# Optimization experiments

Hardware: AMD Instinct MI355X
Metric: run time of the kernel (lower is better)

Reference implementation:

```python
import jax, jax.numpy as jnp
import numpy as np

N = 50000      # nodes
E = 800000     # edges (before self loops)
IN, H, OUT = 128, 64, 64
NEG_SLOPE = 0.2  # PyG GATConv leaky_relu slope


def _glorot(k, shape):
    lim = float(np.sqrt(6.0 / (shape[0] + shape[1])))
    return jax.random.uniform(k, shape, jnp.float32, -lim, lim)


def setup_inputs() -> dict:
    key = jax.random.key(0)
    ks = jax.random.split(key, 16)
    x = jax.random.normal(ks[0], (N, IN), jnp.float32)
    edge_src = jax.random.randint(ks[1], (E,), 0, N, jnp.int32)
    edge_dst = jax.random.randint(ks[2], (E,), 0, N, jnp.int32)
    dims = [(IN, H), (H, H), (H, OUT)]
    inp = {"x": x, "edge_src": edge_src, "edge_dst": edge_dst}
    i = 3
    for l, (di, do) in enumerate(dims):
        inp[f"W{l}"] = _glorot(ks[i], (di, do)); i += 1
        inp[f"as{l}"] = _glorot(ks[i], (1, do))[0]; i += 1
        inp[f"ad{l}"] = _glorot(ks[i], (1, do))[0]; i += 1
        inp[f"b{l}"] = jnp.zeros((do,), jnp.float32)
    return inp


def _gat_layer(x, W, a_src, a_dst, b, src, dst):
    # single-head GATConv (PyG semantics, self loops already in src/dst)
    h = x @ W                              # [N, do]
    s = h @ a_src                          # [N] source attention logits
    d = h @ a_dst                          # [N] dest attention logits
    e = jax.nn.leaky_relu(s[src] + d[dst], NEG_SLOPE)   # [E']
    # segment softmax over incoming edges of each destination node
    m = jax.ops.segment_max(e, dst, num_segments=N)
    w = jnp.exp(e - m[dst])
    denom = jax.ops.segment_sum(w, dst, num_segments=N)
    coef = w / (denom[dst] + 1e-16)
    out = jax.ops.segment_sum(h[src] * coef[:, None], dst, num_segments=N)
    return out + b


def reference(x, edge_src, edge_dst, W0, as0, ad0, b0, W1, as1, ad1, b1, W2, as2, ad2, b2):
    # add self loops (GATConv default add_self_loops=True)
    loop = jnp.arange(N, dtype=edge_src.dtype)
    src = jnp.concatenate([edge_src, loop])
    dst = jnp.concatenate([edge_dst, loop])
    h = jax.nn.relu(_gat_layer(x, W0, as0, ad0, b0, src, dst))
    # dropout is identity in eval mode
    h = jax.nn.relu(_gat_layer(h, W1, as1, ad1, b1, src, dst))
    return _gat_layer(h, W2, as2, ad2, b2, src, dst)
```

## Files before the change

kernel.cpp:

```cpp
#include <hip/hip_runtime.h>
#include <math.h>

#define WAVE 64
#define NEG_SLOPE 0.2f


__global__ __launch_bounds__(256) void bucket_count_kernel(
    const int* __restrict__ dst, int* __restrict__ gcnt, int e, int nb) {
    extern __shared__ int cnt[];
    for (int b = threadIdx.x; b < nb; b += 256) cnt[b] = 0;
    __syncthreads();
    int base = blockIdx.x * 4096;
#pragma unroll
    for (int k = 0; k < 16; ++k) {
        int i = base + k * 256 + threadIdx.x;
        if (i < e) atomicAdd(&cnt[dst[i] >> 7], 1);
    }
    __syncthreads();
    for (int b = threadIdx.x; b < nb; b += 256) {
        int c = cnt[b];
        if (c) atomicAdd(&gcnt[b], c);
    }
}

__global__ __launch_bounds__(512) void bucket_scan_kernel(
    const int* __restrict__ gcnt, int* __restrict__ boff, int* __restrict__ gfill,
    int* __restrict__ rowptr, int nb, int e, int n) {
    __shared__ int sh[512];
    int t = threadIdx.x;
    int v = (t < nb) ? gcnt[t] : 0;
    sh[t] = v;
    __syncthreads();
    for (int o = 1; o < 512; o <<= 1) {
        int u = (t >= o) ? sh[t - o] : 0;
        __syncthreads();
        sh[t] += u;
        __syncthreads();
    }
    if (t < nb) { int ex = sh[t] - v; boff[t] = ex; gfill[t] = ex; }
    if (t == 0) { boff[nb] = e; rowptr[n] = e + n; }
}

__global__ __launch_bounds__(256) void bucket_place_kernel(
    const int* __restrict__ src, const int* __restrict__ dst,
    int* __restrict__ gfill, int2* __restrict__ binned, int e, int nb) {
    extern __shared__ int lds[];
    int* cnt = lds;
    int* bas = lds + nb;
    for (int b = threadIdx.x; b < nb; b += 256) cnt[b] = 0;
    __syncthreads();
    int base = blockIdx.x * 4096;
#pragma unroll
    for (int k = 0; k < 16; ++k) {
        int i = base + k * 256 + threadIdx.x;
        if (i < e) atomicAdd(&cnt[dst[i] >> 7], 1);
    }
    __syncthreads();
    for (int b = threadIdx.x; b < nb; b += 256) {
        int c = cnt[b];
        bas[b] = c ? atomicAdd(&gfill[b], c) : 0;
        cnt[b] = 0;
    }
    __syncthreads();
#pragma unroll
    for (int k = 0; k < 16; ++k) {
        int i = base + k * 256 + threadIdx.x;
        if (i < e) {
            int d = dst[i];
            int bk = d >> 7;
            int r = atomicAdd(&cnt[bk], 1);
            binned[bas[bk] + r] = make_int2(src[i], d);
        }
    }
}

__global__ __launch_bounds__(256) void bucket_build_kernel(
    const int2* __restrict__ binned, const int* __restrict__ boff,
    int* __restrict__ csr_src, int* __restrict__ rowptr, int n) {
    __shared__ int cnt[128], off[128], pcnt[128];
    int b = blockIdx.x;
    int t = threadIdx.x;
    int nodeBase = b << 7;
    int nc = min(128, n - nodeBase);
    int e0 = boff[b], e1 = boff[b + 1];
    int ne = e1 - e0;
    if (t < 128) { cnt[t] = 1; pcnt[t] = 1; }
    __syncthreads();
    for (int i = t; i < ne; i += 256)
        atomicAdd(&cnt[binned[e0 + i].y - nodeBase], 1);
    __syncthreads();
    if (t < 128) off[t] = cnt[t];
    __syncthreads();
    for (int o = 1; o < 128; o <<= 1) {
        int u = (t >= o && t < 128) ? off[t - o] : 0;
        __syncthreads();
        if (t < 128) off[t] += u;
        __syncthreads();
    }
    if (t < 128) off[t] -= cnt[t];
    __syncthreads();
    int csrBase = e0 + nodeBase;
    if (t < nc) {
        rowptr[nodeBase + t] = csrBase + off[t];
        csr_src[csrBase + off[t]] = nodeBase + t;
    }
    for (int i = t; i < ne; i += 256) {
        int2 p = binned[e0 + i];
        int loc = p.y - nodeBase;
        int r = atomicAdd(&pcnt[loc], 1);
        csr_src[csrBase + off[loc] + r] = p.x;
    }
}


template <int K>
__global__ __launch_bounds__(256) void gemm_feat_kernel(
    const float* __restrict__ X, const float* __restrict__ W,
    const float* __restrict__ a_s, const float* __restrict__ a_d,
    float* __restrict__ H, float* __restrict__ S, float* __restrict__ D, int n) {
    constexpr int LSTR = 68;
    __shared__ float Xs[64 * LSTR];
    __shared__ float Ws[64 * LSTR];
    int t = threadIdx.x;
    int tx = t & 15;
    int ty = t >> 4;
    int base = blockIdx.x * 64;
    float acc[4][4] = {};

    int q = t & 3;
    int srow = t >> 2;

    for (int k0 = 0; k0 < K; k0 += 64) {
        int grow = base + srow;
#pragma unroll
        for (int j = 0; j < 4; ++j) {
            int c = 16 * j + 4 * q;
            float4 v = make_float4(0.f, 0.f, 0.f, 0.f);
            if (grow < n) v = *(const float4*)(X + (size_t)grow * K + k0 + c);
            *(float4*)(Xs + srow * LSTR + c) = v;
            float4 w = *(const float4*)(W + (size_t)(k0 + srow) * 64 + c);
            *(float4*)(Ws + srow * LSTR + c) = w;
        }
        __syncthreads();
#pragma unroll 8
        for (int kk = 0; kk < 64; ++kk) {
            float4 wv = *(const float4*)(Ws + kk * LSTR + 4 * tx);
#pragma unroll
            for (int i = 0; i < 4; ++i) {
                float xv = Xs[(4 * ty + i) * LSTR + kk];
                acc[i][0] = fmaf(xv, wv.x, acc[i][0]);
                acc[i][1] = fmaf(xv, wv.y, acc[i][1]);
                acc[i][2] = fmaf(xv, wv.z, acc[i][2]);
                acc[i][3] = fmaf(xv, wv.w, acc[i][3]);
            }
        }
        __syncthreads();
    }

    const float4 av_s = *(const float4*)(a_s + 4 * tx);
    const float4 av_d = *(const float4*)(a_d + 4 * tx);
#pragma unroll
    for (int i = 0; i < 4; ++i) {
        int row = base + 4 * ty + i;
        bool ok = row < n;
        if (ok) {
            float4 hv = make_float4(acc[i][0], acc[i][1], acc[i][2], acc[i][3]);
            *(float4*)(H + (size_t)row * 64 + 4 * tx) = hv;
        }
        float ps = acc[i][0] * av_s.x + acc[i][1] * av_s.y +
                   acc[i][2] * av_s.z + acc[i][3] * av_s.w;
        float pd = acc[i][0] * av_d.x + acc[i][1] * av_d.y +
                   acc[i][2] * av_d.z + acc[i][3] * av_d.w;
        for (int o = 1; o < 16; o <<= 1) {
            ps += __shfl_xor(ps, o);
            pd += __shfl_xor(pd, o);
        }
        if (tx == 0 && ok) { S[row] = ps; D[row] = pd; }
    }
}


__global__ __launch_bounds__(256) void gat_aggregate_kernel(
    const float* __restrict__ H, const float* __restrict__ S,
    const float* __restrict__ D, const int* __restrict__ rowptr,
    const int* __restrict__ csr_src, const float* __restrict__ bias,
    float* __restrict__ OUT, int n, int do_relu) {
    int wid  = (blockIdx.x * blockDim.x + threadIdx.x) >> 6;
    int lane = threadIdx.x & 63;
    if (wid >= n) return;
    int eg = lane >> 4;
    int cg = lane & 15;
    int start = rowptr[wid];
    int end   = rowptr[wid + 1];
    float d_i = D[wid];

    float z = 0.f;
    float4 acc = make_float4(0.f, 0.f, 0.f, 0.f);

    for (int cb = start; cb < end; cb += WAVE) {
        int j = cb + lane;
        bool v = j < end;
        int sc = v ? csr_src[j] : 0;
        float sv = S[sc];
        float e = sv + d_i;
        e = (e > 0.f) ? e : NEG_SLOPE * e;
        float w = v ? __expf(e) : 0.f;

        int nch = min(WAVE, end - cb);
        int rounds = (nch + 3) >> 2;
#pragma unroll 4
        for (int r = 0; r < rounds; ++r) {
            int idx = 4 * r + eg;
            float wr = __shfl(w, idx);
            int   sr = __shfl(sc, idx);
            const float4 hv = *(const float4*)(H + (size_t)sr * 64 + 4 * cg);
            z += wr;
            acc.x = fmaf(wr, hv.x, acc.x);
            acc.y = fmaf(wr, hv.y, acc.y);
            acc.z = fmaf(wr, hv.z, acc.z);
            acc.w = fmaf(wr, hv.w, acc.w);
        }
    }

    for (int o = 16; o < 64; o <<= 1) {
        acc.x += __shfl_xor(acc.x, o);
        acc.y += __shfl_xor(acc.y, o);
        acc.z += __shfl_xor(acc.z, o);
        acc.w += __shfl_xor(acc.w, o);
        z     += __shfl_xor(z, o);
    }

    if (eg == 0) {
        float inv = 1.f / (z + 1e-16f);
        const float4 bv = *(const float4*)(bias + 4 * cg);
        float4 o4;
        o4.x = acc.x * inv + bv.x;
        o4.y = acc.y * inv + bv.y;
        o4.z = acc.z * inv + bv.z;
        o4.w = acc.w * inv + bv.w;
        if (do_relu) {
            o4.x = fmaxf(o4.x, 0.f); o4.y = fmaxf(o4.y, 0.f);
            o4.z = fmaxf(o4.z, 0.f); o4.w = fmaxf(o4.w, 0.f);
        }
        *(float4*)(OUT + (size_t)wid * 64 + 4 * cg) = o4;
    }
}


static inline size_t align256(size_t x) { return (x + 255) & ~(size_t)255; }

extern "C" void kernel_launch(void* const* d_in, const int* in_sizes, int n_in,
                              void* d_out, int out_size, void* d_ws, size_t ws_size,
                              hipStream_t stream) {
    const float* x    = (const float*)d_in[0];
    const int*   esrc = (const int*)d_in[1];
    const int*   edst = (const int*)d_in[2];
    const int E = in_sizes[1];
    const int N = in_sizes[0] / 128;

    const float* W0 = (const float*)d_in[3];
    const float* as0 = (const float*)d_in[4];
    const float* ad0 = (const float*)d_in[5];
    const float* b0 = (const float*)d_in[6];
    const float* W1 = (const float*)d_in[7];
    const float* as1 = (const float*)d_in[8];
    const float* ad1 = (const float*)d_in[9];
    const float* b1 = (const float*)d_in[10];
    const float* W2 = (const float*)d_in[11];
    const float* as2 = (const float*)d_in[12];
    const float* ad2 = (const float*)d_in[13];
    const float* b2 = (const float*)d_in[14];

    const int NB = (N + 127) >> 7;

    char* p = (char*)d_ws;
    int* gcnt    = (int*)p; p += align256((size_t)(NB + 1) * 4);
    int* boff    = (int*)p; p += align256((size_t)(NB + 1) * 4);
    int* gfill   = (int*)p; p += align256((size_t)(NB + 1) * 4);
    int* rowptr  = (int*)p; p += align256((size_t)(N + 1) * 4);
    int* csr_src = (int*)p; p += align256((size_t)(E + N) * 4);
    float* h  = (float*)p; p += align256((size_t)N * 64 * 4);
    float* s  = (float*)p; p += align256((size_t)N * 4);
    float* d  = (float*)p; p += align256((size_t)N * 4);
    float* XA = (float*)p; p += align256((size_t)N * 64 * 4);
    float* XB = (float*)p; p += align256((size_t)N * 64 * 4);
    float* out = (float*)d_out;
    int2* binned = (int2*)XA;

    int nchunk = (E + 4095) / 4096;
    hipMemsetAsync(gcnt, 0, (size_t)(NB + 1) * 4, stream);
    bucket_count_kernel<<<nchunk, 256, NB * 4, stream>>>(edst, gcnt, E, NB);
    bucket_scan_kernel<<<1, 512, 0, stream>>>(gcnt, boff, gfill, rowptr, NB, E, N);
    bucket_place_kernel<<<nchunk, 256, 2 * NB * 4, stream>>>(esrc, edst, gfill, binned, E, NB);
    bucket_build_kernel<<<NB, 256, 0, stream>>>(binned, boff, csr_src, rowptr, N);

    int gemm_grid = (N + 63) / 64;
    int agg_grid  = (N + 3) / 4;

    gemm_feat_kernel<128><<<gemm_grid, 256, 0, stream>>>(x, W0, as0, ad0, h, s, d, N);
    gat_aggregate_kernel<<<agg_grid, 256, 0, stream>>>(h, s, d, rowptr, csr_src, b0, XA, N, 1);

    gemm_feat_kernel<64><<<gemm_grid, 256, 0, stream>>>(XA, W1, as1, ad1, h, s, d, N);
    gat_aggregate_kernel<<<agg_grid, 256, 0, stream>>>(h, s, d, rowptr, csr_src, b1, XB, N, 1);

    gemm_feat_kernel<64><<<gemm_grid, 256, 0, stream>>>(XB, W2, as2, ad2, h, s, d, N);
    gat_aggregate_kernel<<<agg_grid, 256, 0, stream>>>(h, s, d, rowptr, csr_src, b2, out, N, 0);
}
```

Before: 290.3 us.

## Fuse GAT aggregation with next layer's feature GEMM in one kernel

Replaces the separate aggregate-then-GEMM kernel pairs for layers 1 and 2 with a fused kernel. Each block aggregates 64 destination nodes into shared memory, then multiplies that tile by the next layer's weights and emits H, S and D. This avoids writing the intermediate activations to global memory and reading them back, and removes two launches. It also double-buffers the h/s/d buffers and gives the binned edges their own workspace. The cost is fewer blocks, each with 4 waves serially handling 16 nodes, which may hurt load balance and latency hiding in the gather phase.

```diff
diff --git a/kernel.cpp b/kernel.cpp
--- a/kernel.cpp
+++ b/kernel.cpp
@@ -3,6 +3,7 @@
 
 #define WAVE 64
 #define NEG_SLOPE 0.2f
+#define LSTR 68
 
 
 __global__ __launch_bounds__(256) void bucket_count_kernel(
@@ -112,82 +113,11 @@
     }
 }
 
-
-template <int K>
-__global__ __launch_bounds__(256) void gemm_feat_kernel(
-    const float* __restrict__ X, const float* __restrict__ W,
-    const float* __restrict__ a_s, const float* __restrict__ a_d,
-    float* __restrict__ H, float* __restrict__ S, float* __restrict__ D, int n) {
-    constexpr int LSTR = 68;
-    __shared__ float Xs[64 * LSTR];
-    __shared__ float Ws[64 * LSTR];
-    int t = threadIdx.x;
-    int tx = t & 15;
-    int ty = t >> 4;
-    int base = blockIdx.x * 64;
-    float acc[4][4] = {};
-
-    int q = t & 3;
-    int srow = t >> 2;
-
-    for (int k0 = 0; k0 < K; k0 += 64) {
-        int grow = base + srow;
-#pragma unroll
-        for (int j = 0; j < 4; ++j) {
-            int c = 16 * j + 4 * q;
-            float4 v = make_float4(0.f, 0.f, 0.f, 0.f);
-            if (grow < n) v = *(const float4*)(X + (size_t)grow * K + k0 + c);
-            *(float4*)(Xs + srow * LSTR + c) = v;
-            float4 w = *(const float4*)(W + (size_t)(k0 + srow) * 64 + c);
-            *(float4*)(Ws + srow * LSTR + c) = w;
-        }
-        __syncthreads();
-#pragma unroll 8
-        for (int kk = 0; kk < 64; ++kk) {
-            float4 wv = *(const float4*)(Ws + kk * LSTR + 4 * tx);
-#pragma unroll
-            for (int i = 0; i < 4; ++i) {
-                float xv = Xs[(4 * ty + i) * LSTR + kk];
-                acc[i][0] = fmaf(xv, wv.x, acc[i][0]);
-                acc[i][1] = fmaf(xv, wv.y, acc[i][1]);
-                acc[i][2] = fmaf(xv, wv.z, acc[i][2]);
-                acc[i][3] = fmaf(xv, wv.w, acc[i][3]);
-            }
-        }
-        __syncthreads();
-    }
-
-    const float4 av_s = *(const float4*)(a_s + 4 * tx);
-    const float4 av_d = *(const float4*)(a_d + 4 * tx);
-#pragma unroll
-    for (int i = 0; i < 4; ++i) {
-        int row = base + 4 * ty + i;
-        bool ok = row < n;
-        if (ok) {
-            float4 hv = make_float4(acc[i][0], acc[i][1], acc[i][2], acc[i][3]);
-            *(float4*)(H + (size_t)row * 64 + 4 * tx) = hv;
-        }
-        float ps = acc[i][0] * av_s.x + acc[i][1] * av_s.y +
-                   acc[i][2] * av_s.z + acc[i][3] * av_s.w;
-        float pd = acc[i][0] * av_d.x + acc[i][1] * av_d.y +
-                   acc[i][2] * av_d.z + acc[i][3] * av_d.w;
-        for (int o = 1; o < 16; o <<= 1) {
-            ps += __shfl_xor(ps, o);
-            pd += __shfl_xor(pd, o);
-        }
-        if (tx == 0 && ok) { S[row] = ps; D[row] = pd; }
-    }
-}
-
-
-__global__ __launch_bounds__(256) void gat_aggregate_kernel(
+__device__ __forceinline__ float4 gat_node(
     const float* __restrict__ H, const float* __restrict__ S,
-    const float* __restrict__ D, const int* __restrict__ rowptr,
-    const int* __restrict__ csr_src, const float* __restrict__ bias,
-    float* __restrict__ OUT, int n, int do_relu) {
-    int wid  = (blockIdx.x * blockDim.x + threadIdx.x) >> 6;
-    int lane = threadIdx.x & 63;
-    if (wid >= n) return;
+    const int* __restrict__ rowptr, const int* __restrict__ csr_src,
+    const float* __restrict__ D, const float4 bv, int wid, int lane,
+    int do_relu) {
     int eg = lane >> 4;
     int cg = lane & 15;
     int start = rowptr[wid];
@@ -213,7 +143,8 @@
             int idx = 4 * r + eg;
             float wr = __shfl(w, idx);
             int   sr = __shfl(sc, idx);
-            const float4 hv = *(const float4*)(H + (size_t)sr * 64 + 4 * cg);
+            float4 hv = make_float4(0.f, 0.f, 0.f, 0.f);
+            if (idx < nch) hv = *(const float4*)(H + (size_t)sr * 64 + 4 * cg);
             z += wr;
             acc.x = fmaf(wr, hv.x, acc.x);
             acc.y = fmaf(wr, hv.y, acc.y);
@@ -230,20 +161,177 @@
         z     += __shfl_xor(z, o);
     }
 
-    if (eg == 0) {
-        float inv = 1.f / (z + 1e-16f);
-        const float4 bv = *(const float4*)(bias + 4 * cg);
-        float4 o4;
-        o4.x = acc.x * inv + bv.x;
-        o4.y = acc.y * inv + bv.y;
-        o4.z = acc.z * inv + bv.z;
-        o4.w = acc.w * inv + bv.w;
-        if (do_relu) {
-            o4.x = fmaxf(o4.x, 0.f); o4.y = fmaxf(o4.y, 0.f);
-            o4.z = fmaxf(o4.z, 0.f); o4.w = fmaxf(o4.w, 0.f);
-        }
-        *(float4*)(OUT + (size_t)wid * 64 + 4 * cg) = o4;
-    }
+    float inv = 1.f / (z + 1e-16f);
+    float4 o4;
+    o4.x = acc.x * inv + bv.x;
+    o4.y = acc.y * inv + bv.y;
+    o4.z = acc.z * inv + bv.z;
+    o4.w = acc.w * inv + bv.w;
+    if (do_relu) {
+        o4.x = fmaxf(o4.x, 0.f); o4.y = fmaxf(o4.y, 0.f);
+        o4.z = fmaxf(o4.z, 0.f); o4.w = fmaxf(o4.w, 0.f);
+    }
+    return o4;
+}
+
+
+__global__ __launch_bounds__(256) void gemm_feat_kernel(
+    const float* __restrict__ X, const float* __restrict__ W,
+    const float* __restrict__ a_s, const float* __restrict__ a_d,
+    float* __restrict__ H, float* __restrict__ S, float* __restrict__ D, int n) {
+    constexpr int K = 128;
+    __shared__ float Xs[64 * LSTR];
+    __shared__ float Ws[64 * LSTR];
+    int t = threadIdx.x;
+    int tx = t & 15;
+    int ty = t >> 4;
+    int base = blockIdx.x * 64;
+    float acc[4][4] = {};
+
+    int q = t & 3;
+    int srow = t >> 2;
+
+    for (int k0 = 0; k0 < K; k0 += 64) {
+        int grow = base + srow;
+#pragma unroll
+        for (int j = 0; j < 4; ++j) {
+            int c = 16 * j + 4 * q;
+            float4 v = make_float4(0.f, 0.f, 0.f, 0.f);
+            if (grow < n) v = *(const float4*)(X + (size_t)grow * K + k0 + c);
+            *(float4*)(Xs + srow * LSTR + c) = v;
+            float4 w = *(const float4*)(W + (size_t)(k0 + srow) * 64 + c);
+            *(float4*)(Ws + srow * LSTR + c) = w;
+        }
+        __syncthreads();
+#pragma unroll 8
+        for (int kk = 0; kk < 64; ++kk) {
+            float4 wv = *(const float4*)(Ws + kk * LSTR + 4 * tx);
+#pragma unroll
+            for (int i = 0; i < 4; ++i) {
+                float xv = Xs[(4 * ty + i) * LSTR + kk];
+                acc[i][0] = fmaf(xv, wv.x, acc[i][0]);
+                acc[i][1] = fmaf(xv, wv.y, acc[i][1]);
+                acc[i][2] = fmaf(xv, wv.z, acc[i][2]);
+                acc[i][3] = fmaf(xv, wv.w, acc[i][3]);
+            }
+        }
+        __syncthreads();
+    }
+
+    const float4 av_s = *(const float4*)(a_s + 4 * tx);
+    const float4 av_d = *(const float4*)(a_d + 4 * tx);
+#pragma unroll
+    for (int i = 0; i < 4; ++i) {
+        int row = base + 4 * ty + i;
+        bool ok = row < n;
+        if (ok) {
+            float4 hv = make_float4(acc[i][0], acc[i][1], acc[i][2], acc[i][3]);
+            *(float4*)(H + (size_t)row * 64 + 4 * tx) = hv;
+        }
+        float ps = acc[i][0] * av_s.x + acc[i][1] * av_s.y +
+                   acc[i][2] * av_s.z + acc[i][3] * av_s.w;
+        float pd = acc[i][0] * av_d.x + acc[i][1] * av_d.y +
+                   acc[i][2] * av_d.z + acc[i][3] * av_d.w;
+        for (int o = 1; o < 16; o <<= 1) {
+            ps += __shfl_xor(ps, o);
+            pd += __shfl_xor(pd, o);
+        }
+        if (tx == 0 && ok) { S[row] = ps; D[row] = pd; }
+    }
+}
+
+
+__global__ __launch_bounds__(256) void agg_gemm_kernel(
+    const float* __restrict__ H, const float* __restrict__ S,
+    const float* __restrict__ D, const int* __restrict__ rowptr,
+    const int* __restrict__ csr_src, const float* __restrict__ bias,
+    const float* __restrict__ W, const float* __restrict__ a_s,
+    const float* __restrict__ a_d, float* __restrict__ Hout,
+    float* __restrict__ Sout, float* __restrict__ Dout, int n) {
+    __shared__ float Xs[64 * LSTR];
+    __shared__ float Ws[64 * LSTR];
+    int t = threadIdx.x;
+    int lane = t & 63;
+    int wv = t >> 6;
+    int base = blockIdx.x * 64;
+
+    {
+        int q = t & 3;
+        int srow = t >> 2;
+#pragma unroll
+        for (int j = 0; j < 4; ++j) {
+            int c = 16 * j + 4 * q;
+            float4 w = *(const float4*)(W + (size_t)srow * 64 + c);
+            *(float4*)(Ws + srow * LSTR + c) = w;
+        }
+    }
+
+    int eg = lane >> 4;
+    int cg = lane & 15;
+    const float4 bv = *(const float4*)(bias + 4 * cg);
+    for (int local = wv; local < 64; local += 4) {
+        int wid = base + local;
+        if (wid < n) {
+            float4 o4 = gat_node(H, S, rowptr, csr_src, D, bv, wid, lane, 1);
+            if (eg == 0) *(float4*)(Xs + local * LSTR + 4 * cg) = o4;
+        } else if (eg == 0) {
+            *(float4*)(Xs + local * LSTR + 4 * cg) = make_float4(0.f, 0.f, 0.f, 0.f);
+        }
+    }
+    __syncthreads();
+
+    int tx = t & 15;
+    int ty = t >> 4;
+    float acc[4][4] = {};
+#pragma unroll 8
+    for (int kk = 0; kk < 64; ++kk) {
+        float4 wvv = *(const float4*)(Ws + kk * LSTR + 4 * tx);
+#pragma unroll
+        for (int i = 0; i < 4; ++i) {
+            float xv = Xs[(4 * ty + i) * LSTR + kk];
+            acc[i][0] = fmaf(xv, wvv.x, acc[i][0]);
+            acc[i][1] = fmaf(xv, wvv.y, acc[i][1]);
+            acc[i][2] = fmaf(xv, wvv.z, acc[i][2]);
+            acc[i][3] = fmaf(xv, wvv.w, acc[i][3]);
+        }
+    }
+
+    const float4 av_s = *(const float4*)(a_s + 4 * tx);
+    const float4 av_d = *(const float4*)(a_d + 4 * tx);
+#pragma unroll
+    for (int i = 0; i < 4; ++i) {
+        int row = base + 4 * ty + i;
+        bool ok = row < n;
+        if (ok) {
+            float4 hv = make_float4(acc[i][0], acc[i][1], acc[i][2], acc[i][3]);
+            *(float4*)(Hout + (size_t)row * 64 + 4 * tx) = hv;
+        }
+        float ps = acc[i][0] * av_s.x + acc[i][1] * av_s.y +
+                   acc[i][2] * av_s.z + acc[i][3] * av_s.w;
+        float pd = acc[i][0] * av_d.x + acc[i][1] * av_d.y +
+                   acc[i][2] * av_d.z + acc[i][3] * av_d.w;
+        for (int o = 1; o < 16; o <<= 1) {
+            ps += __shfl_xor(ps, o);
+            pd += __shfl_xor(pd, o);
+        }
+        if (tx == 0 && ok) { Sout[row] = ps; Dout[row] = pd; }
+    }
+}
+
+
+__global__ __launch_bounds__(256) void gat_aggregate_kernel(
+    const float* __restrict__ H, const float* __restrict__ S,
+    const float* __restrict__ D, const int* __restrict__ rowptr,
+    const int* __restrict__ csr_src, const float* __restrict__ bias,
+    float* __restrict__ OUT, int n) {
+    int wid  = (blockIdx.x * blockDim.x + threadIdx.x) >> 6;
+    int lane = threadIdx.x & 63;
+    if (wid >= n) return;
+    int eg = lane >> 4;
+    int cg = lane & 15;
+    const float4 bv = *(const float4*)(bias + 4 * cg);
+    float4 o4 = gat_node(H, S, rowptr, csr_src, D, bv, wid, lane, 0);
+    if (eg == 0) *(float4*)(OUT + (size_t)wid * 64 + 4 * cg) = o4;
 }
 
 
@@ -279,13 +367,14 @@
     int* gfill   = (int*)p; p += align256((size_t)(NB + 1) * 4);
     int* rowptr  = (int*)p; p += align256((size_t)(N + 1) * 4);
     int* csr_src = (int*)p; p += align256((size_t)(E + N) * 4);
-    float* h  = (float*)p; p += align256((size_t)N * 64 * 4);
-    float* s  = (float*)p; p += align256((size_t)N * 4);
-    float* d  = (float*)p; p += align256((size_t)N * 4);
-    float* XA = (float*)p; p += align256((size_t)N * 64 * 4);
-    float* XB = (float*)p; p += align256((size_t)N * 64 * 4);
+    int2* binned = (int2*)p; p += align256((size_t)E * 8);
+    float* hA = (float*)p; p += align256((size_t)N * 64 * 4);
+    float* hB = (float*)p; p += align256((size_t)N * 64 * 4);
+    float* sA = (float*)p; p += align256((size_t)N * 4);
+    float* dA = (float*)p; p += align256((size_t)N * 4);
+    float* sB = (float*)p; p += align256((size_t)N * 4);
+    float* dB = (float*)p; p += align256((size_t)N * 4);
     float* out = (float*)d_out;
-    int2* binned = (int2*)XA;
 
     int nchunk = (E + 4095) / 4096;
     hipMemsetAsync(gcnt, 0, (size_t)(NB + 1) * 4, stream);
@@ -294,15 +383,13 @@
     bucket_place_kernel<<<nchunk, 256, 2 * NB * 4, stream>>>(esrc, edst, gfill, binned, E, NB);
     bucket_build_kernel<<<NB, 256, 0, stream>>>(binned, boff, csr_src, rowptr, N);
 
-    int gemm_grid = (N + 63) / 64;
+    int tile_grid = (N + 63) / 64;
     int agg_grid  = (N + 3) / 4;
 
-    gemm_feat_kernel<128><<<gemm_grid, 256, 0, stream>>>(x, W0, as0, ad0, h, s, d, N);
-    gat_aggregate_kernel<<<agg_grid, 256, 0, stream>>>(h, s, d, rowptr, csr_src, b0, XA, N, 1);
-
-    gemm_feat_kernel<64><<<gemm_grid, 256, 0, stream>>>(XA, W1, as1, ad1, h, s, d, N);
-    gat_aggregate_kernel<<<agg_grid, 256, 0, stream>>>(h, s, d, rowptr, csr_src, b1, XB, N, 1);
-
-    gemm_feat_kernel<64><<<gemm_grid, 256, 0, stream>>>(XB, W2, as2, ad2, h, s, d, N);
-    gat_aggregate_kernel<<<agg_grid, 256, 0, stream>>>(h, s, d, rowptr, csr_src, b2, out, N, 0);
-}
+    gemm_feat_kernel<<<tile_grid, 256, 0, stream>>>(x, W0, as0, ad0, hA, sA, dA, N);
+    agg_gemm_kernel<<<tile_grid, 256, 0, stream>>>(hA, sA, dA, rowptr, csr_src, b0,
+                                                   W1, as1, ad1, hB, sB, dB, N);
+    agg_gemm_kernel<<<tile_grid, 256, 0, stream>>>(hB, sB, dB, rowptr, csr_src, b1,
+                                                   W2, as2, ad2, hA, sA, dA, N);
+    gat_aggregate_kernel<<<agg_grid, 256, 0, stream>>>(hA, sA, dA, rowptr, csr_src, b2, out, N);
+}
```

Measured after the change: 305.0 us. +5.1%, slower.
